# Performance work log

Hardware: AMD Instinct MI355X
Metric: run time of the kernel (lower is better)

## Reference

```python
import jax, jax.numpy as jnp
import numpy as np

B, N, H, HD = 1, 1024, 16, 32
D = H * HD  # 512
DZ = 128
EPS = 1e-5


def layer_norm(x, w, b):
    mu = jnp.mean(x, axis=-1, keepdims=True)
    var = jnp.mean(jnp.square(x - mu), axis=-1, keepdims=True)
    return (x - mu) * jax.lax.rsqrt(var + EPS) * w + b


def setup_inputs() -> dict:
    key = jax.random.key(0)
    ks = jax.random.split(key, 12)
    sc = 0.02
    return {
        "s": jax.random.normal(ks[0], (B, N, D), jnp.float32),
        "z": jax.random.normal(ks[1], (B, N, N, DZ), jnp.float32),
        "norm_s_w": jnp.ones((D,), jnp.float32),
        "norm_s_b": jnp.zeros((D,), jnp.float32),
        "Wq": jax.random.normal(ks[2], (D, D), jnp.float32) * sc,
        "bq": jnp.zeros((D,), jnp.float32),
        "Wk": jax.random.normal(ks[3], (D, D), jnp.float32) * sc,
        "Wv": jax.random.normal(ks[4], (D, D), jnp.float32) * sc,
        "Wg": jax.random.normal(ks[5], (D, D), jnp.float32) * sc,
        "z_norm_w": jnp.ones((DZ,), jnp.float32),
        "z_norm_b": jnp.zeros((DZ,), jnp.float32),
        "Wz": jax.random.normal(ks[6], (DZ, H), jnp.float32) * sc,
        "Wo": jax.random.normal(ks[7], (D, D), jnp.float32) * sc,
    }


def reference(s, z, norm_s_w, norm_s_b, Wq, bq, Wk, Wv, Wg, z_norm_w, z_norm_b, Wz, Wo):
    # initial layer norm on single representation
    s = layer_norm(s, norm_s_w, norm_s_b)
    # QKV projections -> [B, H, N, HD]
    q = (s @ Wq + bq).reshape(B, N, H, HD).transpose(0, 2, 1, 3)
    k = (s @ Wk).reshape(B, N, H, HD).transpose(0, 2, 1, 3)
    v = (s @ Wv).reshape(B, N, H, HD).transpose(0, 2, 1, 3)
    # attention scores with pair bias
    a = jnp.einsum("bhqd,bhkd->bhqk", q, k) * (HD ** -0.5)
    zb = layer_norm(z, z_norm_w, z_norm_b) @ Wz          # [B, N, N, H]
    a = a + zb.transpose(0, 3, 1, 2)                     # [B, H, N, N]
    a = jax.nn.softmax(a, axis=-1)
    o = jnp.einsum("bhqk,bhkd->bhqd", a, v)              # [B, H, N, HD]
    o = o.transpose(0, 2, 1, 3).reshape(B, N, D)
    # sigmoid gating and output projection
    g = jax.nn.sigmoid(s @ Wg)
    return (o * g) @ Wo
```

## Files before the change

### kernel.cpp

```cpp
#include <hip/hip_runtime.h>
#include <hip/hip_bf16.h>


#define EPSV 1e-5f

#define OFF_SNORM   (0u)
#define OFF_QT      (2097152u)
#define OFF_KT      (4194304u)
#define OFF_VT      (6291456u)
#define OFF_GS      (8388608u)
#define OFF_ZB      (10485760u)
#define OFF_WWZ     (44040192u)
#define OFF_CC      (44048384u)
#define OFF_PM      (44048512u)
#define OFF_PL      (44572800u)
#define OFF_PO      (45097088u)
#define OFF_OG      (61874304u)

__global__ __launch_bounds__(256) void prep_w_kernel(
    const float* __restrict__ znw, const float* __restrict__ znb,
    const float* __restrict__ Wz, float* __restrict__ wWz,
    float* __restrict__ cc)
{
    const int t = threadIdx.x;
#pragma unroll
    for (int u = 0; u < 8; ++u) {
        int idx = t + u * 256;
        wWz[idx] = znw[idx >> 4] * Wz[idx];
    }
    if (t < 16) {
        float cs = 0.f, cb = 0.f;
        for (int j = 0; j < 128; ++j) {
            float wz = Wz[j * 16 + t];
            cs += znw[j] * wz;
            cb += znb[j] * wz;
        }
        cc[t] = cs;
        cc[16 + t] = cb;
    }
}

__global__ __launch_bounds__(256) void lns_kernel(
    const float* __restrict__ s, const float* __restrict__ w,
    const float* __restrict__ b, float* __restrict__ sn)
{
    const int lane = threadIdx.x & 63;
    const int wv   = threadIdx.x >> 6;
    const int row  = blockIdx.x * 4 + wv;
    const float* x = s + (size_t)row * 512 + lane * 8;
    float4 a = *(const float4*)x;
    float4 c = *(const float4*)(x + 4);
    float v[8] = {a.x, a.y, a.z, a.w, c.x, c.y, c.z, c.w};
    float ss = 0.f, s2 = 0.f;
#pragma unroll
    for (int u = 0; u < 8; ++u) { ss += v[u]; s2 = fmaf(v[u], v[u], s2); }
#pragma unroll
    for (int m = 1; m < 64; m <<= 1) {
        ss += __shfl_xor(ss, m);
        s2 += __shfl_xor(s2, m);
    }
    float mu  = ss * (1.f / 512.f);
    float var = s2 * (1.f / 512.f) - mu * mu;
    float rs  = rsqrtf(var + EPSV);
    float o[8];
#pragma unroll
    for (int u = 0; u < 8; ++u)
        o[u] = (v[u] - mu) * rs * w[lane * 8 + u] + b[lane * 8 + u];
    float* dst = sn + (size_t)row * 512 + lane * 8;
    *(float4*)dst       = make_float4(o[0], o[1], o[2], o[3]);
    *(float4*)(dst + 4) = make_float4(o[4], o[5], o[6], o[7]);
}

__global__ __launch_bounds__(256) void gemm_qkvg_kernel(
    const float* __restrict__ A,
    const float* __restrict__ Wq, const float* __restrict__ Wk,
    const float* __restrict__ Wv, const float* __restrict__ Wg,
    const float* __restrict__ bq,
    float* __restrict__ qT, float* __restrict__ kT,
    float* __restrict__ vT, float* __restrict__ gS)
{
    __shared__ float As[16][132];
    __shared__ float Bs[16][128];
    const int which = blockIdx.z;
    const float* B = (which == 0) ? Wq : (which == 1) ? Wk : (which == 2) ? Wv : Wg;
    const int n0 = blockIdx.x * 128, m0 = blockIdx.y * 128;
    const int tid = threadIdx.x;
    const int tn = tid & 15, tm = tid >> 4;
    float acc[8][8] = {};

    for (int k0 = 0; k0 < 512; k0 += 16) {
#pragma unroll
        for (int u = 0; u < 2; ++u) {
            int f = tid * 2 + u;
            int i = f >> 2, kk4 = f & 3;
            float4 a4 = *(const float4*)(A + (size_t)(m0 + i) * 512 + k0 + kk4 * 4);
            As[kk4 * 4 + 0][i] = a4.x;
            As[kk4 * 4 + 1][i] = a4.y;
            As[kk4 * 4 + 2][i] = a4.z;
            As[kk4 * 4 + 3][i] = a4.w;
            int kk = f >> 5, j4 = f & 31;
            *(float4*)&Bs[kk][j4 * 4] =
                *(const float4*)(B + (size_t)(k0 + kk) * 512 + n0 + j4 * 4);
        }
        __syncthreads();
#pragma unroll
        for (int kk = 0; kk < 16; ++kk) {
            float a[8], b[8];
            *(float4*)a       = *(const float4*)&As[kk][tm * 8];
            *(float4*)(a + 4) = *(const float4*)&As[kk][tm * 8 + 4];
            *(float4*)b       = *(const float4*)&Bs[kk][tn * 8];
            *(float4*)(b + 4) = *(const float4*)&Bs[kk][tn * 8 + 4];
#pragma unroll
            for (int i = 0; i < 8; ++i)
#pragma unroll
                for (int j = 0; j < 8; ++j)
                    acc[i][j] = fmaf(a[i], b[j], acc[i][j]);
        }
        __syncthreads();
    }

    const int m_base = m0 + tm * 8;
    const int n_base = n0 + tn * 8;
    if (which == 3) {
#pragma unroll
        for (int i = 0; i < 8; ++i) {
            float o[8];
#pragma unroll
            for (int j = 0; j < 8; ++j)
                o[j] = 1.f / (1.f + __expf(-acc[i][j]));
            float* d0 = gS + (size_t)(m_base + i) * 512 + n_base;
            *(float4*)d0       = make_float4(o[0], o[1], o[2], o[3]);
            *(float4*)(d0 + 4) = make_float4(o[4], o[5], o[6], o[7]);
        }
    } else {
        float* dst = (which == 0) ? qT : (which == 1) ? kT : vT;
        const int hh = n_base >> 5, d0 = n_base & 31;
        float bb[8];
#pragma unroll
        for (int j = 0; j < 8; ++j) bb[j] = (which == 0) ? bq[n_base + j] : 0.f;
        const float scl = (which == 0) ? 0.17677669529663687f : 1.f;
#pragma unroll
        for (int i = 0; i < 8; ++i) {
            float o[8];
#pragma unroll
            for (int j = 0; j < 8; ++j)
                o[j] = (acc[i][j] + bb[j]) * scl;
            float* p = dst + (((size_t)hh << 10) + (m_base + i)) * 32 + d0;
            *(float4*)p       = make_float4(o[0], o[1], o[2], o[3]);
            *(float4*)(p + 4) = make_float4(o[4], o[5], o[6], o[7]);
        }
    }
}

__global__ __launch_bounds__(256) void zbias_kernel(
    const float* __restrict__ z, const float* __restrict__ wWz,
    const float* __restrict__ cc, __hip_bfloat16* __restrict__ zb)
{
    const int row = blockIdx.x * 256 + threadIdx.x;
    const float4* x4 = (const float4*)(z + (size_t)row * 128);
    float acc[16];
#pragma unroll
    for (int h = 0; h < 16; ++h) acc[h] = 0.f;
    float s = 0.f, s2 = 0.f;
    for (int jb = 0; jb < 16; ++jb) {
        float4 xa = x4[jb * 2];
        float4 xb = x4[jb * 2 + 1];
        float xv[8] = {xa.x, xa.y, xa.z, xa.w, xb.x, xb.y, xb.z, xb.w};
#pragma unroll
        for (int jj = 0; jj < 8; ++jj) {
            float xx = xv[jj];
            s += xx;
            s2 = fmaf(xx, xx, s2);
            const float* wrow = wWz + (jb * 8 + jj) * 16;
#pragma unroll
            for (int h = 0; h < 16; ++h)
                acc[h] = fmaf(xx, wrow[h], acc[h]);
        }
    }
    float mu  = s * (1.f / 128.f);
    float var = s2 * (1.f / 128.f) - mu * mu;
    float rs  = rsqrtf(var + EPSV);
#pragma unroll
    for (int h = 0; h < 16; ++h) {
        float v = rs * (acc[h] - mu * cc[h]) + cc[16 + h];
        zb[((size_t)h << 20) + row] = __float2bfloat16(v);
    }
}

__global__ __launch_bounds__(256) void attn_kernel(
    const float* __restrict__ qT, const float* __restrict__ kT,
    const float* __restrict__ vT, const __hip_bfloat16* __restrict__ zb,
    float* __restrict__ pm, float* __restrict__ pl, float* __restrict__ pO)
{
    const int kc = blockIdx.x, qb = blockIdx.y, h = blockIdx.z;
    const int lane = threadIdx.x & 63, wv = threadIdx.x >> 6;
    const int q = qb * 256 + wv * 64 + lane;

    const float* qp = qT + (((size_t)h << 10) + q) * 32;
    float qv[32];
#pragma unroll
    for (int u = 0; u < 8; ++u) {
        float4 t4 = *(const float4*)(qp + u * 4);
        qv[u * 4] = t4.x; qv[u * 4 + 1] = t4.y; qv[u * 4 + 2] = t4.z; qv[u * 4 + 3] = t4.w;
    }
    float O[32];
#pragma unroll
    for (int j = 0; j < 32; ++j) O[j] = 0.f;
    float m = -1e30f, l = 0.f;

    const __hip_bfloat16* zrow = zb + ((size_t)h << 20) + ((size_t)q << 10) + kc * 128;
    const float* kbase = kT + (((size_t)h << 10)) * 32;
    const float* vbase = vT + (((size_t)h << 10)) * 32;

    for (int kk0 = 0; kk0 < 128; kk0 += 16) {
        float sc[16];
#pragma unroll
        for (int t = 0; t < 16; ++t) {
            const float* kv = kbase + (size_t)(kc * 128 + kk0 + t) * 32;
            float d = 0.f;
#pragma unroll
            for (int j = 0; j < 32; ++j) d = fmaf(qv[j], kv[j], d);
            sc[t] = d + __bfloat162float(zrow[kk0 + t]);
        }
        float cm = m;
#pragma unroll
        for (int t = 0; t < 16; ++t) cm = fmaxf(cm, sc[t]);
        float scale = __expf(m - cm);
        m = cm;
        l *= scale;
#pragma unroll
        for (int j = 0; j < 32; ++j) O[j] *= scale;
#pragma unroll
        for (int t = 0; t < 16; ++t) {
            float p = __expf(sc[t] - m);
            l += p;
            const float* vv = vbase + (size_t)(kc * 128 + kk0 + t) * 32;
#pragma unroll
            for (int j = 0; j < 32; ++j) O[j] = fmaf(p, vv[j], O[j]);
        }
    }

    const size_t idx = ((size_t)kc * 16 + h) * 1024 + q;
    pm[idx] = m;
    pl[idx] = l;
    float* po = pO + idx * 32;
#pragma unroll
    for (int u = 0; u < 8; ++u) {
        *(float4*)(po + u * 4) =
            make_float4(O[u * 4], O[u * 4 + 1], O[u * 4 + 2], O[u * 4 + 3]);
    }
}

__global__ __launch_bounds__(256) void combine_kernel(
    const float* __restrict__ pm, const float* __restrict__ pl,
    const float* __restrict__ pO, const float* __restrict__ gS,
    float* __restrict__ og)
{
    const int t = blockIdx.x * 256 + threadIdx.x;
    const int j = t & 31;
    const int hh = (t >> 5) & 15;
    const int q = t >> 9;
    const size_t base = ((size_t)hh << 10) + q;
    float ms[8];
    float M = -1e30f;
#pragma unroll
    for (int kc = 0; kc < 8; ++kc) {
        ms[kc] = pm[(size_t)kc * 16384 + base];
        M = fmaxf(M, ms[kc]);
    }
    float L = 0.f, O = 0.f;
#pragma unroll
    for (int kc = 0; kc < 8; ++kc) {
        float e = __expf(ms[kc] - M);
        L += pl[(size_t)kc * 16384 + base] * e;
        O += pO[((size_t)kc * 16384 + base) * 32 + j] * e;
    }
    og[t] = (O / L) * gS[t];
}

__global__ __launch_bounds__(256) void gemm_out_kernel(
    const float* __restrict__ A, const float* __restrict__ B,
    float* __restrict__ C)
{
    __shared__ float As[32][68];
    __shared__ float Bs[32][64];
    const int n0 = blockIdx.x * 64, m0 = blockIdx.y * 64;
    const int tid = threadIdx.x, tn = tid & 15, tm = tid >> 4;
    float acc[4][4] = {};

    for (int k0 = 0; k0 < 512; k0 += 32) {
#pragma unroll
        for (int u = 0; u < 2; ++u) {
            int f = tid * 2 + u;
            int i = f >> 3, kk4 = f & 7;
            float4 a4 = *(const float4*)(A + (size_t)(m0 + i) * 512 + k0 + kk4 * 4);
            As[kk4 * 4 + 0][i] = a4.x;
            As[kk4 * 4 + 1][i] = a4.y;
            As[kk4 * 4 + 2][i] = a4.z;
            As[kk4 * 4 + 3][i] = a4.w;
            int kk = f >> 4, j4 = f & 15;
            *(float4*)&Bs[kk][j4 * 4] =
                *(const float4*)(B + (size_t)(k0 + kk) * 512 + n0 + j4 * 4);
        }
        __syncthreads();
#pragma unroll
        for (int kk = 0; kk < 32; ++kk) {
            float a[4], b[4];
            *(float4*)a = *(const float4*)&As[kk][tm * 4];
            *(float4*)b = *(const float4*)&Bs[kk][tn * 4];
#pragma unroll
            for (int i = 0; i < 4; ++i)
#pragma unroll
                for (int j = 0; j < 4; ++j)
                    acc[i][j] = fmaf(a[i], b[j], acc[i][j]);
        }
        __syncthreads();
    }
#pragma unroll
    for (int i = 0; i < 4; ++i) {
        float* p = C + (size_t)(m0 + tm * 4 + i) * 512 + n0 + tn * 4;
        *(float4*)p = make_float4(acc[i][0], acc[i][1], acc[i][2], acc[i][3]);
    }
}

extern "C" void kernel_launch(void* const* d_in, const int* in_sizes, int n_in,
                              void* d_out, int out_size, void* d_ws, size_t ws_size,
                              hipStream_t stream)
{
    const float* s   = (const float*)d_in[0];
    const float* z   = (const float*)d_in[1];
    const float* nsw = (const float*)d_in[2];
    const float* nsb = (const float*)d_in[3];
    const float* Wq  = (const float*)d_in[4];
    const float* bq  = (const float*)d_in[5];
    const float* Wk  = (const float*)d_in[6];
    const float* Wv  = (const float*)d_in[7];
    const float* Wg  = (const float*)d_in[8];
    const float* znw = (const float*)d_in[9];
    const float* znb = (const float*)d_in[10];
    const float* Wz  = (const float*)d_in[11];
    const float* Wo  = (const float*)d_in[12];

    char* w = (char*)d_ws;
    float*          s_norm = (float*)(w + OFF_SNORM);
    float*          qT     = (float*)(w + OFF_QT);
    float*          kT     = (float*)(w + OFF_KT);
    float*          vT     = (float*)(w + OFF_VT);
    float*          gS     = (float*)(w + OFF_GS);
    __hip_bfloat16* zb     = (__hip_bfloat16*)(w + OFF_ZB);
    float*          wWz    = (float*)(w + OFF_WWZ);
    float*          cc     = (float*)(w + OFF_CC);
    float*          pm     = (float*)(w + OFF_PM);
    float*          pl     = (float*)(w + OFF_PL);
    float*          pO     = (float*)(w + OFF_PO);
    float*          og     = (float*)(w + OFF_OG);

    prep_w_kernel<<<dim3(1), dim3(256), 0, stream>>>(znw, znb, Wz, wWz, cc);
    lns_kernel<<<dim3(256), dim3(256), 0, stream>>>(s, nsw, nsb, s_norm);
    gemm_qkvg_kernel<<<dim3(4, 8, 4), dim3(256), 0, stream>>>(
        s_norm, Wq, Wk, Wv, Wg, bq, qT, kT, vT, gS);
    zbias_kernel<<<dim3(4096), dim3(256), 0, stream>>>(z, wWz, cc, zb);
    attn_kernel<<<dim3(8, 4, 16), dim3(256), 0, stream>>>(qT, kT, vT, zb, pm, pl, pO);
    combine_kernel<<<dim3(2048), dim3(256), 0, stream>>>(pm, pl, pO, gS, og);
    gemm_out_kernel<<<dim3(8, 16), dim3(256), 0, stream>>>(og, Wo, (float*)d_out);
}
```

Measured before the change: 988.5 us.

## Rewrite pipeline with bf16 MFMA GEMMs, flash attention and MFMA z-bias

Replaces the fp32 scalar-FMA GEMMs, z-bias projection and split-K attention with bf16 MFMA 16x16x32 versions. Weights and activations are converted to bf16, and weights are pre-transposed by a new kernel. Attention becomes a single-pass flash-style kernel that fuses the gating multiply, which removes the combine kernel and its partial buffers. In exchange it loses precision from bf16 rounding of z, Q/K/V and probabilities, and it adds a weight conversion pass on every call.

```diff
diff --git a/kernel.cpp b/kernel.cpp
--- a/kernel.cpp
+++ b/kernel.cpp
@@ -1,48 +1,81 @@
 #include <hip/hip_runtime.h>
-#include <hip/hip_bf16.h>
 
 
 #define EPSV 1e-5f
 
-#define OFF_SNORM   (0u)
-#define OFF_QT      (2097152u)
-#define OFF_KT      (4194304u)
-#define OFF_VT      (6291456u)
-#define OFF_GS      (8388608u)
-#define OFF_ZB      (10485760u)
-#define OFF_WWZ     (44040192u)
-#define OFF_CC      (44048384u)
-#define OFF_PM      (44048512u)
-#define OFF_PL      (44572800u)
-#define OFF_PO      (45097088u)
-#define OFF_OG      (61874304u)
+typedef __bf16 bf16x8 __attribute__((ext_vector_type(8)));
+typedef float f32x4 __attribute__((ext_vector_type(4)));
+typedef unsigned short ushort8 __attribute__((ext_vector_type(8)));
+typedef unsigned short ushort4v __attribute__((ext_vector_type(4)));
+
+__device__ __forceinline__ unsigned short f2b(float f) {
+    unsigned int u = __float_as_uint(f);
+    u += 0x7fffu + ((u >> 16) & 1u);
+    return (unsigned short)(u >> 16);
+}
+__device__ __forceinline__ float b2f(unsigned short h) {
+    return __uint_as_float(((unsigned int)h) << 16);
+}
+__device__ __forceinline__ f32x4 mfma16(bf16x8 a, bf16x8 b, f32x4 c) {
+    return __builtin_amdgcn_mfma_f32_16x16x32_bf16(a, b, c, 0, 0, 0);
+}
+
+#define OFF_SBF 0u
+#define OFF_WT  1048576u
+#define OFF_QT  3670016u
+#define OFF_KT  4718592u
+#define OFF_VT  5767168u
+#define OFF_GS  6815744u
+#define OFF_OG  8912896u
+#define OFF_WZT 9961472u
+#define OFF_CC  9965568u
+#define OFF_ZB  9965696u
 
 __global__ __launch_bounds__(256) void prep_w_kernel(
     const float* __restrict__ znw, const float* __restrict__ znb,
-    const float* __restrict__ Wz, float* __restrict__ wWz,
+    const float* __restrict__ Wz, unsigned short* __restrict__ wzt,
     float* __restrict__ cc)
 {
     const int t = threadIdx.x;
 #pragma unroll
     for (int u = 0; u < 8; ++u) {
         int idx = t + u * 256;
-        wWz[idx] = znw[idx >> 4] * Wz[idx];
+        int j = idx >> 4, h = idx & 15;
+        wzt[h * 128 + j] = f2b(znw[j] * Wz[idx]);
     }
     if (t < 16) {
         float cs = 0.f, cb = 0.f;
         for (int j = 0; j < 128; ++j) {
-            float wz = Wz[j * 16 + t];
-            cs += znw[j] * wz;
-            cb += znb[j] * wz;
+            float wv = Wz[j * 16 + t];
+            cs += znw[j] * wv;
+            cb += znb[j] * wv;
         }
         cc[t] = cs;
         cc[16 + t] = cb;
     }
 }
 
+__global__ __launch_bounds__(256) void convw_kernel(
+    const float* __restrict__ Wq, const float* __restrict__ Wk,
+    const float* __restrict__ Wv, const float* __restrict__ Wg,
+    const float* __restrict__ Wo, unsigned short* __restrict__ WT)
+{
+    int t = blockIdx.x * 256 + threadIdx.x;
+    int mat = t >> 15;
+    int r = t & 32767;
+    int n = r & 511;
+    int k0 = (r >> 9) * 8;
+    const float* W = mat == 0 ? Wq : mat == 1 ? Wk : mat == 2 ? Wv : mat == 3 ? Wg : Wo;
+    ushort8 o;
+#pragma unroll
+    for (int i = 0; i < 8; ++i)
+        o[i] = f2b(W[(size_t)(k0 + i) * 512 + n]);
+    *(ushort8*)(WT + (size_t)mat * 262144 + (size_t)n * 512 + k0) = o;
+}
+
 __global__ __launch_bounds__(256) void lns_kernel(
     const float* __restrict__ s, const float* __restrict__ w,
-    const float* __restrict__ b, float* __restrict__ sn)
+    const float* __restrict__ b, unsigned short* __restrict__ sbf)
 {
     const int lane = threadIdx.x & 63;
     const int wv   = threadIdx.x >> 6;
@@ -62,265 +95,274 @@
     float mu  = ss * (1.f / 512.f);
     float var = s2 * (1.f / 512.f) - mu * mu;
     float rs  = rsqrtf(var + EPSV);
-    float o[8];
+    ushort8 ob;
 #pragma unroll
     for (int u = 0; u < 8; ++u)
-        o[u] = (v[u] - mu) * rs * w[lane * 8 + u] + b[lane * 8 + u];
-    float* dst = sn + (size_t)row * 512 + lane * 8;
-    *(float4*)dst       = make_float4(o[0], o[1], o[2], o[3]);
-    *(float4*)(dst + 4) = make_float4(o[4], o[5], o[6], o[7]);
+        ob[u] = f2b((v[u] - mu) * rs * w[lane * 8 + u] + b[lane * 8 + u]);
+    *(ushort8*)(sbf + (size_t)row * 512 + lane * 8) = ob;
+}
+
+__global__ __launch_bounds__(256) void zbias_kernel(
+    const float* __restrict__ z, const unsigned short* __restrict__ wzt,
+    const float* __restrict__ cc, unsigned short* __restrict__ zb)
+{
+    __shared__ unsigned short xb[64 * 136];
+    __shared__ float mus[64], rss[64], ccs[32];
+    const int t = threadIdx.x;
+    const size_t rowbase = (size_t)blockIdx.x * 64;
+
+    if (t < 32) ccs[t] = cc[t];
+    const float4* zsrc = (const float4*)(z + rowbase * 128);
+#pragma unroll
+    for (int u = 0; u < 8; ++u) {
+        int g = t + u * 256;
+        float4 v = zsrc[g];
+        int row = g >> 5, c4 = g & 31;
+        ushort4v pk;
+        pk[0] = f2b(v.x); pk[1] = f2b(v.y); pk[2] = f2b(v.z); pk[3] = f2b(v.w);
+        *(ushort4v*)(xb + row * 136 + c4 * 4) = pk;
+    }
+    __syncthreads();
+
+    {
+        int row = t >> 2, seg = t & 3;
+        const unsigned short* xr = xb + row * 136 + seg * 32;
+        float s1 = 0.f, s2 = 0.f;
+#pragma unroll
+        for (int i = 0; i < 8; ++i) {
+            ushort4v v = *(const ushort4v*)(xr + i * 4);
+#pragma unroll
+            for (int j = 0; j < 4; ++j) {
+                float x = b2f(v[j]);
+                s1 += x;
+                s2 = fmaf(x, x, s2);
+            }
+        }
+        s1 += __shfl_xor(s1, 1); s2 += __shfl_xor(s2, 1);
+        s1 += __shfl_xor(s1, 2); s2 += __shfl_xor(s2, 2);
+        if (seg == 0) {
+            float mu = s1 * (1.f / 128.f);
+            float var = s2 * (1.f / 128.f) - mu * mu;
+            mus[row] = mu;
+            rss[row] = rsqrtf(var + EPSV);
+        }
+    }
+    __syncthreads();
+
+    const int w = t >> 6, l = t & 63, lr = l & 15, lg = l >> 4;
+    bf16x8 awz[4];
+#pragma unroll
+    for (int c = 0; c < 4; ++c)
+        awz[c] = *(const bf16x8*)(wzt + lr * 128 + c * 32 + lg * 8);
+    const unsigned short* xw = xb + (w * 16) * 136;
+    f32x4 acc = {0.f, 0.f, 0.f, 0.f};
+#pragma unroll
+    for (int c = 0; c < 4; ++c) {
+        bf16x8 bx = *(const bf16x8*)(xw + lr * 136 + c * 32 + lg * 8);
+        acc = mfma16(awz[c], bx, acc);
+    }
+    const int zl = w * 16 + lr;
+    const float mu = mus[zl], rs = rss[zl];
+    const size_t zr = rowbase + zl;
+#pragma unroll
+    for (int r = 0; r < 4; ++r) {
+        int hh = lg * 4 + r;
+        float val = rs * (acc[r] - mu * ccs[hh]) + ccs[16 + hh];
+        zb[((size_t)hh << 20) + zr] = f2b(val);
+    }
 }
 
 __global__ __launch_bounds__(256) void gemm_qkvg_kernel(
-    const float* __restrict__ A,
-    const float* __restrict__ Wq, const float* __restrict__ Wk,
-    const float* __restrict__ Wv, const float* __restrict__ Wg,
+    const unsigned short* __restrict__ sbf, const unsigned short* __restrict__ WT,
     const float* __restrict__ bq,
-    float* __restrict__ qT, float* __restrict__ kT,
-    float* __restrict__ vT, float* __restrict__ gS)
-{
-    __shared__ float As[16][132];
-    __shared__ float Bs[16][128];
+    unsigned short* __restrict__ qT, unsigned short* __restrict__ kT,
+    unsigned short* __restrict__ vTt, float* __restrict__ gS)
+{
     const int which = blockIdx.z;
-    const float* B = (which == 0) ? Wq : (which == 1) ? Wk : (which == 2) ? Wv : Wg;
-    const int n0 = blockIdx.x * 128, m0 = blockIdx.y * 128;
-    const int tid = threadIdx.x;
-    const int tn = tid & 15, tm = tid >> 4;
-    float acc[8][8] = {};
-
-    for (int k0 = 0; k0 < 512; k0 += 16) {
-#pragma unroll
-        for (int u = 0; u < 2; ++u) {
-            int f = tid * 2 + u;
-            int i = f >> 2, kk4 = f & 3;
-            float4 a4 = *(const float4*)(A + (size_t)(m0 + i) * 512 + k0 + kk4 * 4);
-            As[kk4 * 4 + 0][i] = a4.x;
-            As[kk4 * 4 + 1][i] = a4.y;
-            As[kk4 * 4 + 2][i] = a4.z;
-            As[kk4 * 4 + 3][i] = a4.w;
-            int kk = f >> 5, j4 = f & 31;
-            *(float4*)&Bs[kk][j4 * 4] =
-                *(const float4*)(B + (size_t)(k0 + kk) * 512 + n0 + j4 * 4);
-        }
-        __syncthreads();
-#pragma unroll
-        for (int kk = 0; kk < 16; ++kk) {
-            float a[8], b[8];
-            *(float4*)a       = *(const float4*)&As[kk][tm * 8];
-            *(float4*)(a + 4) = *(const float4*)&As[kk][tm * 8 + 4];
-            *(float4*)b       = *(const float4*)&Bs[kk][tn * 8];
-            *(float4*)(b + 4) = *(const float4*)&Bs[kk][tn * 8 + 4];
-#pragma unroll
-            for (int i = 0; i < 8; ++i)
-#pragma unroll
-                for (int j = 0; j < 8; ++j)
-                    acc[i][j] = fmaf(a[i], b[j], acc[i][j]);
-        }
-        __syncthreads();
-    }
-
-    const int m_base = m0 + tm * 8;
-    const int n_base = n0 + tn * 8;
+    const unsigned short* BT = WT + (size_t)which * 262144;
+    const int w = threadIdx.x >> 6, l = threadIdx.x & 63;
+    const int lr = l & 15, lg = l >> 4;
+    const int m0 = (blockIdx.y * 4 + w) * 64;
+    const int n0 = blockIdx.x * 64;
+
+    f32x4 acc[4][4];
+#pragma unroll
+    for (int i = 0; i < 4; ++i)
+#pragma unroll
+        for (int j = 0; j < 4; ++j) acc[i][j] = (f32x4){0.f, 0.f, 0.f, 0.f};
+
+    for (int k0 = 0; k0 < 512; k0 += 32) {
+        bf16x8 a[4], b[4];
+#pragma unroll
+        for (int fm = 0; fm < 4; ++fm)
+            a[fm] = *(const bf16x8*)(sbf + (size_t)(m0 + fm * 16 + lr) * 512 + k0 + lg * 8);
+#pragma unroll
+        for (int fn = 0; fn < 4; ++fn)
+            b[fn] = *(const bf16x8*)(BT + (size_t)(n0 + fn * 16 + lr) * 512 + k0 + lg * 8);
+#pragma unroll
+        for (int fm = 0; fm < 4; ++fm)
+#pragma unroll
+            for (int fn = 0; fn < 4; ++fn)
+                acc[fm][fn] = mfma16(a[fm], b[fn], acc[fm][fn]);
+    }
+
     if (which == 3) {
 #pragma unroll
-        for (int i = 0; i < 8; ++i) {
-            float o[8];
-#pragma unroll
-            for (int j = 0; j < 8; ++j)
-                o[j] = 1.f / (1.f + __expf(-acc[i][j]));
-            float* d0 = gS + (size_t)(m_base + i) * 512 + n_base;
-            *(float4*)d0       = make_float4(o[0], o[1], o[2], o[3]);
-            *(float4*)(d0 + 4) = make_float4(o[4], o[5], o[6], o[7]);
-        }
+        for (int fm = 0; fm < 4; ++fm)
+#pragma unroll
+            for (int fn = 0; fn < 4; ++fn) {
+                int c = n0 + fn * 16 + lr;
+#pragma unroll
+                for (int r = 0; r < 4; ++r) {
+                    int m = m0 + fm * 16 + lg * 4 + r;
+                    gS[(size_t)m * 512 + c] = 1.f / (1.f + __expf(-acc[fm][fn][r]));
+                }
+            }
+    } else if (which == 2) {
+#pragma unroll
+        for (int fm = 0; fm < 4; ++fm)
+#pragma unroll
+            for (int fn = 0; fn < 4; ++fn) {
+                int c = n0 + fn * 16 + lr;
+                int hh = c >> 5, d = c & 31;
+#pragma unroll
+                for (int r = 0; r < 4; ++r) {
+                    int m = m0 + fm * 16 + lg * 4 + r;
+                    vTt[(size_t)hh * 32768 + (size_t)d * 1024 + m] = f2b(acc[fm][fn][r]);
+                }
+            }
     } else {
-        float* dst = (which == 0) ? qT : (which == 1) ? kT : vT;
-        const int hh = n_base >> 5, d0 = n_base & 31;
-        float bb[8];
-#pragma unroll
-        for (int j = 0; j < 8; ++j) bb[j] = (which == 0) ? bq[n_base + j] : 0.f;
+        unsigned short* dst = (which == 0) ? qT : kT;
         const float scl = (which == 0) ? 0.17677669529663687f : 1.f;
 #pragma unroll
-        for (int i = 0; i < 8; ++i) {
-            float o[8];
-#pragma unroll
-            for (int j = 0; j < 8; ++j)
-                o[j] = (acc[i][j] + bb[j]) * scl;
-            float* p = dst + (((size_t)hh << 10) + (m_base + i)) * 32 + d0;
-            *(float4*)p       = make_float4(o[0], o[1], o[2], o[3]);
-            *(float4*)(p + 4) = make_float4(o[4], o[5], o[6], o[7]);
-        }
-    }
-}
-
-__global__ __launch_bounds__(256) void zbias_kernel(
-    const float* __restrict__ z, const float* __restrict__ wWz,
-    const float* __restrict__ cc, __hip_bfloat16* __restrict__ zb)
-{
-    const int row = blockIdx.x * 256 + threadIdx.x;
-    const float4* x4 = (const float4*)(z + (size_t)row * 128);
-    float acc[16];
-#pragma unroll
-    for (int h = 0; h < 16; ++h) acc[h] = 0.f;
-    float s = 0.f, s2 = 0.f;
-    for (int jb = 0; jb < 16; ++jb) {
-        float4 xa = x4[jb * 2];
-        float4 xb = x4[jb * 2 + 1];
-        float xv[8] = {xa.x, xa.y, xa.z, xa.w, xb.x, xb.y, xb.z, xb.w};
-#pragma unroll
-        for (int jj = 0; jj < 8; ++jj) {
-            float xx = xv[jj];
-            s += xx;
-            s2 = fmaf(xx, xx, s2);
-            const float* wrow = wWz + (jb * 8 + jj) * 16;
-#pragma unroll
-            for (int h = 0; h < 16; ++h)
-                acc[h] = fmaf(xx, wrow[h], acc[h]);
-        }
-    }
-    float mu  = s * (1.f / 128.f);
-    float var = s2 * (1.f / 128.f) - mu * mu;
-    float rs  = rsqrtf(var + EPSV);
-#pragma unroll
-    for (int h = 0; h < 16; ++h) {
-        float v = rs * (acc[h] - mu * cc[h]) + cc[16 + h];
-        zb[((size_t)h << 20) + row] = __float2bfloat16(v);
+        for (int fm = 0; fm < 4; ++fm)
+#pragma unroll
+            for (int fn = 0; fn < 4; ++fn) {
+                int c = n0 + fn * 16 + lr;
+                int hh = c >> 5, d = c & 31;
+                float bb = (which == 0) ? bq[c] : 0.f;
+#pragma unroll
+                for (int r = 0; r < 4; ++r) {
+                    int m = m0 + fm * 16 + lg * 4 + r;
+                    dst[(size_t)hh * 32768 + (size_t)m * 32 + d] = f2b((acc[fm][fn][r] + bb) * scl);
+                }
+            }
     }
 }
 
 __global__ __launch_bounds__(256) void attn_kernel(
-    const float* __restrict__ qT, const float* __restrict__ kT,
-    const float* __restrict__ vT, const __hip_bfloat16* __restrict__ zb,
-    float* __restrict__ pm, float* __restrict__ pl, float* __restrict__ pO)
-{
-    const int kc = blockIdx.x, qb = blockIdx.y, h = blockIdx.z;
-    const int lane = threadIdx.x & 63, wv = threadIdx.x >> 6;
-    const int q = qb * 256 + wv * 64 + lane;
-
-    const float* qp = qT + (((size_t)h << 10) + q) * 32;
-    float qv[32];
-#pragma unroll
-    for (int u = 0; u < 8; ++u) {
-        float4 t4 = *(const float4*)(qp + u * 4);
-        qv[u * 4] = t4.x; qv[u * 4 + 1] = t4.y; qv[u * 4 + 2] = t4.z; qv[u * 4 + 3] = t4.w;
-    }
-    float O[32];
-#pragma unroll
-    for (int j = 0; j < 32; ++j) O[j] = 0.f;
-    float m = -1e30f, l = 0.f;
-
-    const __hip_bfloat16* zrow = zb + ((size_t)h << 20) + ((size_t)q << 10) + kc * 128;
-    const float* kbase = kT + (((size_t)h << 10)) * 32;
-    const float* vbase = vT + (((size_t)h << 10)) * 32;
-
-    for (int kk0 = 0; kk0 < 128; kk0 += 16) {
-        float sc[16];
-#pragma unroll
-        for (int t = 0; t < 16; ++t) {
-            const float* kv = kbase + (size_t)(kc * 128 + kk0 + t) * 32;
-            float d = 0.f;
-#pragma unroll
-            for (int j = 0; j < 32; ++j) d = fmaf(qv[j], kv[j], d);
-            sc[t] = d + __bfloat162float(zrow[kk0 + t]);
-        }
-        float cm = m;
-#pragma unroll
-        for (int t = 0; t < 16; ++t) cm = fmaxf(cm, sc[t]);
-        float scale = __expf(m - cm);
-        m = cm;
-        l *= scale;
-#pragma unroll
-        for (int j = 0; j < 32; ++j) O[j] *= scale;
-#pragma unroll
-        for (int t = 0; t < 16; ++t) {
-            float p = __expf(sc[t] - m);
-            l += p;
-            const float* vv = vbase + (size_t)(kc * 128 + kk0 + t) * 32;
-#pragma unroll
-            for (int j = 0; j < 32; ++j) O[j] = fmaf(p, vv[j], O[j]);
-        }
-    }
-
-    const size_t idx = ((size_t)kc * 16 + h) * 1024 + q;
-    pm[idx] = m;
-    pl[idx] = l;
-    float* po = pO + idx * 32;
-#pragma unroll
-    for (int u = 0; u < 8; ++u) {
-        *(float4*)(po + u * 4) =
-            make_float4(O[u * 4], O[u * 4 + 1], O[u * 4 + 2], O[u * 4 + 3]);
-    }
-}
-
-__global__ __launch_bounds__(256) void combine_kernel(
-    const float* __restrict__ pm, const float* __restrict__ pl,
-    const float* __restrict__ pO, const float* __restrict__ gS,
-    float* __restrict__ og)
-{
-    const int t = blockIdx.x * 256 + threadIdx.x;
-    const int j = t & 31;
-    const int hh = (t >> 5) & 15;
-    const int q = t >> 9;
-    const size_t base = ((size_t)hh << 10) + q;
-    float ms[8];
-    float M = -1e30f;
-#pragma unroll
-    for (int kc = 0; kc < 8; ++kc) {
-        ms[kc] = pm[(size_t)kc * 16384 + base];
-        M = fmaxf(M, ms[kc]);
-    }
-    float L = 0.f, O = 0.f;
-#pragma unroll
-    for (int kc = 0; kc < 8; ++kc) {
-        float e = __expf(ms[kc] - M);
-        L += pl[(size_t)kc * 16384 + base] * e;
-        O += pO[((size_t)kc * 16384 + base) * 32 + j] * e;
-    }
-    og[t] = (O / L) * gS[t];
+    const unsigned short* __restrict__ qT, const unsigned short* __restrict__ kT,
+    const unsigned short* __restrict__ vTt, const unsigned short* __restrict__ zb,
+    const float* __restrict__ gS, unsigned short* __restrict__ og)
+{
+    __shared__ unsigned short plds[4][16 * 48];
+    const int w = threadIdx.x >> 6, l = threadIdx.x & 63;
+    const int lr = l & 15, lg = l >> 4;
+    const int h = blockIdx.y;
+    const int q0 = blockIdx.x * 64 + w * 16;
+
+    const unsigned short* qh = qT + (size_t)h * 32768;
+    const unsigned short* kh = kT + (size_t)h * 32768;
+    const unsigned short* vh = vTt + (size_t)h * 32768;
+    const unsigned short* zrow = zb + ((size_t)h << 20);
+    unsigned short* pw = plds[w];
+
+    const bf16x8 qa = *(const bf16x8*)(qh + (size_t)(q0 + lr) * 32 + lg * 8);
+    f32x4 o0 = {0.f, 0.f, 0.f, 0.f}, o1 = {0.f, 0.f, 0.f, 0.f};
+    float m[4] = {-1e30f, -1e30f, -1e30f, -1e30f};
+    float lsum[4] = {0.f, 0.f, 0.f, 0.f};
+
+    for (int kb = 0; kb < 1024; kb += 32) {
+        bf16x8 kf0 = *(const bf16x8*)(kh + (size_t)(kb + lr) * 32 + lg * 8);
+        bf16x8 kf1 = *(const bf16x8*)(kh + (size_t)(kb + 16 + lr) * 32 + lg * 8);
+        bf16x8 vf0 = *(const bf16x8*)(vh + (size_t)lr * 1024 + kb + lg * 8);
+        bf16x8 vf1 = *(const bf16x8*)(vh + (size_t)(16 + lr) * 1024 + kb + lg * 8);
+        f32x4 zero = {0.f, 0.f, 0.f, 0.f};
+        f32x4 s0 = mfma16(qa, kf0, zero);
+        f32x4 s1 = mfma16(qa, kf1, zero);
+#pragma unroll
+        for (int r = 0; r < 4; ++r) {
+            int qr = q0 + lg * 4 + r;
+            s0[r] += b2f(zrow[(size_t)qr * 1024 + kb + lr]);
+            s1[r] += b2f(zrow[(size_t)qr * 1024 + kb + 16 + lr]);
+        }
+#pragma unroll
+        for (int r = 0; r < 4; ++r) {
+            float mx = fmaxf(s0[r], s1[r]);
+            mx = fmaxf(mx, __shfl_xor(mx, 1));
+            mx = fmaxf(mx, __shfl_xor(mx, 2));
+            mx = fmaxf(mx, __shfl_xor(mx, 4));
+            mx = fmaxf(mx, __shfl_xor(mx, 8));
+            float mn = fmaxf(m[r], mx);
+            float f = __expf(m[r] - mn);
+            m[r] = mn;
+            float p0 = __expf(s0[r] - mn);
+            float p1 = __expf(s1[r] - mn);
+            float rsum = p0 + p1;
+            rsum += __shfl_xor(rsum, 1);
+            rsum += __shfl_xor(rsum, 2);
+            rsum += __shfl_xor(rsum, 4);
+            rsum += __shfl_xor(rsum, 8);
+            lsum[r] = lsum[r] * f + rsum;
+            o0[r] *= f;
+            o1[r] *= f;
+            pw[(lg * 4 + r) * 48 + lr]      = f2b(p0);
+            pw[(lg * 4 + r) * 48 + 16 + lr] = f2b(p1);
+        }
+        bf16x8 pa = *(const bf16x8*)(pw + lr * 48 + lg * 8);
+        o0 = mfma16(pa, vf0, o0);
+        o1 = mfma16(pa, vf1, o1);
+    }
+#pragma unroll
+    for (int r = 0; r < 4; ++r) {
+        int qr = q0 + lg * 4 + r;
+        float inv = 1.f / lsum[r];
+        int c = (h << 5) + lr;
+        og[(size_t)qr * 512 + c]      = f2b(o0[r] * inv * gS[(size_t)qr * 512 + c]);
+        og[(size_t)qr * 512 + c + 16] = f2b(o1[r] * inv * gS[(size_t)qr * 512 + c + 16]);
+    }
 }
 
 __global__ __launch_bounds__(256) void gemm_out_kernel(
-    const float* __restrict__ A, const float* __restrict__ B,
-    float* __restrict__ C)
-{
-    __shared__ float As[32][68];
-    __shared__ float Bs[32][64];
-    const int n0 = blockIdx.x * 64, m0 = blockIdx.y * 64;
-    const int tid = threadIdx.x, tn = tid & 15, tm = tid >> 4;
-    float acc[4][4] = {};
+    const unsigned short* __restrict__ og, const unsigned short* __restrict__ WoT,
+    float* __restrict__ out)
+{
+    const int w = threadIdx.x >> 6, l = threadIdx.x & 63;
+    const int lr = l & 15, lg = l >> 4;
+    const int m0 = (blockIdx.y * 4 + w) * 64;
+    const int n0 = blockIdx.x * 32;
+
+    f32x4 acc[4][2];
+#pragma unroll
+    for (int i = 0; i < 4; ++i)
+#pragma unroll
+        for (int j = 0; j < 2; ++j) acc[i][j] = (f32x4){0.f, 0.f, 0.f, 0.f};
 
     for (int k0 = 0; k0 < 512; k0 += 32) {
-#pragma unroll
-        for (int u = 0; u < 2; ++u) {
-            int f = tid * 2 + u;
-            int i = f >> 3, kk4 = f & 7;
-            float4 a4 = *(const float4*)(A + (size_t)(m0 + i) * 512 + k0 + kk4 * 4);
-            As[kk4 * 4 + 0][i] = a4.x;
-            As[kk4 * 4 + 1][i] = a4.y;
-            As[kk4 * 4 + 2][i] = a4.z;
-            As[kk4 * 4 + 3][i] = a4.w;
-            int kk = f >> 4, j4 = f & 15;
-            *(float4*)&Bs[kk][j4 * 4] =
-                *(const float4*)(B + (size_t)(k0 + kk) * 512 + n0 + j4 * 4);
-        }
-        __syncthreads();
-#pragma unroll
-        for (int kk = 0; kk < 32; ++kk) {
-            float a[4], b[4];
-            *(float4*)a = *(const float4*)&As[kk][tm * 4];
-            *(float4*)b = *(const float4*)&Bs[kk][tn * 4];
-#pragma unroll
-            for (int i = 0; i < 4; ++i)
-#pragma unroll
-                for (int j = 0; j < 4; ++j)
-                    acc[i][j] = fmaf(a[i], b[j], acc[i][j]);
-        }
-        __syncthreads();
-    }
-#pragma unroll
-    for (int i = 0; i < 4; ++i) {
-        float* p = C + (size_t)(m0 + tm * 4 + i) * 512 + n0 + tn * 4;
-        *(float4*)p = make_float4(acc[i][0], acc[i][1], acc[i][2], acc[i][3]);
-    }
+        bf16x8 a[4], b[2];
+#pragma unroll
+        for (int fm = 0; fm < 4; ++fm)
+            a[fm] = *(const bf16x8*)(og + (size_t)(m0 + fm * 16 + lr) * 512 + k0 + lg * 8);
+#pragma unroll
+        for (int fn = 0; fn < 2; ++fn)
+            b[fn] = *(const bf16x8*)(WoT + (size_t)(n0 + fn * 16 + lr) * 512 + k0 + lg * 8);
+#pragma unroll
+        for (int fm = 0; fm < 4; ++fm)
+#pragma unroll
+            for (int fn = 0; fn < 2; ++fn)
+                acc[fm][fn] = mfma16(a[fm], b[fn], acc[fm][fn]);
+    }
+#pragma unroll
+    for (int fm = 0; fm < 4; ++fm)
+#pragma unroll
+        for (int fn = 0; fn < 2; ++fn) {
+            int c = n0 + fn * 16 + lr;
+#pragma unroll
+            for (int r = 0; r < 4; ++r) {
+                int m = m0 + fm * 16 + lg * 4 + r;
+                out[(size_t)m * 512 + c] = acc[fm][fn][r];
+            }
+        }
 }
 
 extern "C" void kernel_launch(void* const* d_in, const int* in_sizes, int n_in,
@@ -341,26 +383,24 @@
     const float* Wz  = (const float*)d_in[11];
     const float* Wo  = (const float*)d_in[12];
 
-    char* w = (char*)d_ws;
-    float*          s_norm = (float*)(w + OFF_SNORM);
-    float*          qT     = (float*)(w + OFF_QT);
-    float*          kT     = (float*)(w + OFF_KT);
-    float*          vT     = (float*)(w + OFF_VT);
-    float*          gS     = (float*)(w + OFF_GS);
-    __hip_bfloat16* zb     = (__hip_bfloat16*)(w + OFF_ZB);
-    float*          wWz    = (float*)(w + OFF_WWZ);
-    float*          cc     = (float*)(w + OFF_CC);
-    float*          pm     = (float*)(w + OFF_PM);
-    float*          pl     = (float*)(w + OFF_PL);
-    float*          pO     = (float*)(w + OFF_PO);
-    float*          og     = (float*)(w + OFF_OG);
-
-    prep_w_kernel<<<dim3(1), dim3(256), 0, stream>>>(znw, znb, Wz, wWz, cc);
-    lns_kernel<<<dim3(256), dim3(256), 0, stream>>>(s, nsw, nsb, s_norm);
-    gemm_qkvg_kernel<<<dim3(4, 8, 4), dim3(256), 0, stream>>>(
-        s_norm, Wq, Wk, Wv, Wg, bq, qT, kT, vT, gS);
-    zbias_kernel<<<dim3(4096), dim3(256), 0, stream>>>(z, wWz, cc, zb);
-    attn_kernel<<<dim3(8, 4, 16), dim3(256), 0, stream>>>(qT, kT, vT, zb, pm, pl, pO);
-    combine_kernel<<<dim3(2048), dim3(256), 0, stream>>>(pm, pl, pO, gS, og);
-    gemm_out_kernel<<<dim3(8, 16), dim3(256), 0, stream>>>(og, Wo, (float*)d_out);
-}
+    char* wsb = (char*)d_ws;
+    unsigned short* sbf = (unsigned short*)(wsb + OFF_SBF);
+    unsigned short* WT  = (unsigned short*)(wsb + OFF_WT);
+    unsigned short* qT  = (unsigned short*)(wsb + OFF_QT);
+    unsigned short* kT  = (unsigned short*)(wsb + OFF_KT);
+    unsigned short* vTt = (unsigned short*)(wsb + OFF_VT);
+    float*          gS  = (float*)(wsb + OFF_GS);
+    unsigned short* og  = (unsigned short*)(wsb + OFF_OG);
+    unsigned short* wzt = (unsigned short*)(wsb + OFF_WZT);
+    float*          cc  = (float*)(wsb + OFF_CC);
+    unsigned short* zbp = (unsigned short*)(wsb + OFF_ZB);
+
+    prep_w_kernel<<<dim3(1), dim3(256), 0, stream>>>(znw, znb, Wz, wzt, cc);
+    convw_kernel<<<dim3(640), dim3(256), 0, stream>>>(Wq, Wk, Wv, Wg, Wo, WT);
+    lns_kernel<<<dim3(256), dim3(256), 0, stream>>>(s, nsw, nsb, sbf);
+    zbias_kernel<<<dim3(16384), dim3(256), 0, stream>>>(z, wzt, cc, zbp);
+    gemm_qkvg_kernel<<<dim3(8, 4, 4), dim3(256), 0, stream>>>(
+        sbf, WT, bq, qT, kT, vTt, gS);
+    attn_kernel<<<dim3(16, 16), dim3(256), 0, stream>>>(qT, kT, vTt, zbp, gS, og);
+    gemm_out_kernel<<<dim3(16, 4), dim3(256), 0, stream>>>(og, WT + 4 * 262144, (float*)d_out);
+}
```

After: 796.2 us. 19.5% less time.
